# Optimization experiments

Measured on AMD Instinct MI355X. Metric: run time of the kernel, lower is better.

Reference implementation:

```python
import jax, jax.numpy as jnp
import numpy as np
from jax.scipy.linalg import solve_triangular

EPS = 2e-05  # module eps (only used on Cholesky failure in torch; cov is PD here since M >> N)


def setup_inputs() -> dict:
    key = jax.random.key(0)
    k1, k2, k3 = jax.random.split(key, 3)
    B, N, H, W = 8, 512, 64, 64
    return {
        "cont_feat": jax.random.normal(k1, (B, N, H, W), dtype=jnp.float32),
        "styl_feat": jax.random.normal(k2, (B, N, H, W), dtype=jnp.float32),
        "x_real": jax.random.normal(k3, (B, N, H, W), dtype=jnp.float32),
    }


def reference(cont_feat, styl_feat, x_real):
    B, N, cH, cW = cont_feat.shape
    xc = cont_feat.reshape(B, N, -1)   # [B, N, Mc]
    xs = styl_feat.reshape(B, N, -1)   # [B, N, Ms]
    # x_real is reshaped in the original but never used by whitening()

    # whitening: center, covariance, Cholesky, inv(L) @ x (as triangular solve)
    xc_c = xc - jnp.mean(xc, axis=-1, keepdims=True)
    cov_c = jnp.einsum('bnm,bkm->bnk', xc_c, xc_c) / (xc_c.shape[-1] - 1)  # [B,N,N]
    Lc = jnp.linalg.cholesky(cov_c)
    whiten = solve_triangular(Lc, xc_c, lower=True)  # == inv(Lc) @ xc_c

    # coloring: style covariance Cholesky, Ls @ whiten + style mean
    xs_mean = jnp.mean(xs, axis=-1, keepdims=True)
    xs_c = xs - xs_mean
    cov_s = jnp.einsum('bnm,bkm->bnk', xs_c, xs_c) / (xs_c.shape[-1] - 1)
    Ls = jnp.linalg.cholesky(cov_s)
    out = jnp.einsum('bnk,bkm->bnm', Ls, whiten) + xs_mean
    return out.reshape(B, N, cH, cW)
```

## Files before the change

kernel.cpp:

```cpp
#include <hip/hip_runtime.h>
#include <stdint.h>


using short8   = __attribute__((ext_vector_type(8))) short;
using short4_t = __attribute__((ext_vector_type(4))) short;
using f32x4    = __attribute__((ext_vector_type(4))) float;

#define DEVI static __device__ __forceinline__

DEVI uint16_t f32_to_bf16(float f) {
  union { float f; uint32_t u; } v{f};
  uint32_t u = v.u;
  return (uint16_t)((u + 0x7fffu + ((u >> 16) & 1u)) >> 16);
}

DEVI f32x4 mfma16(short8 a, short8 b, f32x4 c) {
  return __builtin_amdgcn_mfma_f32_16x16x32_bf16(a, b, c, 0, 0, 0);
}

typedef __attribute__((address_space(3))) uint32_t lds_u32;
typedef __attribute__((address_space(1))) const uint32_t gmem_u32;

DEVI void async_cp16(const uint16_t* g, uint16_t* l) {
  __builtin_amdgcn_global_load_lds((gmem_u32*)g, (lds_u32*)l, 16, 0, 0);
}

DEVI void stage_tile(const uint16_t* __restrict__ src, int stride,
                     uint16_t* lds, int tid) {
  int w64 = (tid >> 6) << 6;
  #pragma unroll
  for (int i = 0; i < 4; ++i) {
    int f = i * 256 + tid;
    int r = f >> 3, s = f & 7;
    int c = s ^ (r & 7);
    async_cp16(src + r * stride + c * 8, lds + (i * 256 + w64) * 8);
  }
}

DEVI short8 frag_ld(const uint16_t* lds, int r, int ch) {
  return *(const short8*)(lds + r * 64 + ((ch ^ (r & 7)) * 8));
}

__global__ __launch_bounds__(256) void k_meanconv(
    const float* __restrict__ cont, const float* __restrict__ styl,
    uint16_t* __restrict__ Yc, uint16_t* __restrict__ Ys, float* __restrict__ mus) {
  int rid = blockIdx.x;
  int row = rid & 4095;
  bool is_s = rid >= 4096;
  const float* src = (is_s ? styl : cont) + (size_t)row * 4096;
  uint16_t* dst = (is_s ? Ys : Yc) + (size_t)row * 4096;
  int tid = threadIdx.x, lane = tid & 63, w = tid >> 6;

  float4 v[4];
  #pragma unroll
  for (int i = 0; i < 4; ++i) v[i] = ((const float4*)src)[i * 256 + tid];
  float s = 0.f;
  #pragma unroll
  for (int i = 0; i < 4; ++i) s += v[i].x + v[i].y + v[i].z + v[i].w;
  #pragma unroll
  for (int off = 32; off > 0; off >>= 1) s += __shfl_down(s, off);
  __shared__ float red[4];
  if (lane == 0) red[w] = s;
  __syncthreads();
  float mean = (red[0] + red[1] + red[2] + red[3]) * (1.0f / 4096.0f);
  if (is_s && tid == 0) mus[row] = mean;

  #pragma unroll
  for (int i = 0; i < 4; ++i) {
    short4_t o;
    o[0] = (short)f32_to_bf16(v[i].x - mean);
    o[1] = (short)f32_to_bf16(v[i].y - mean);
    o[2] = (short)f32_to_bf16(v[i].z - mean);
    o[3] = (short)f32_to_bf16(v[i].w - mean);
    ((short4_t*)dst)[i * 256 + tid] = o;
  }
}

__global__ __launch_bounds__(256) void k_covp(const uint16_t* __restrict__ Y,
                                              float* __restrict__ covA,
                                              float* __restrict__ covB) {
  int bx = blockIdx.x;
  int split = bx & 1, rest = bx >> 1;
  int mat = rest / 10, q = rest % 10;
  int it = (q >= 6) ? 3 : (q >= 3) ? 2 : (q >= 1) ? 1 : 0;
  int jt = q - it * (it + 1) / 2;
  const uint16_t* A = Y + (size_t)mat * 2097152;
  float* C = covA + (size_t)mat * 262144;
  __shared__ uint16_t Al[128 * 64], Bl[128 * 64];
  int tid = threadIdx.x, lane = tid & 63, w = tid >> 6;
  int wr = w >> 1, wc = w & 1, m16 = lane & 15, q4 = lane >> 4;

  f32x4 acc[4][4] = {};
  for (int kb = split * 32; kb < split * 32 + 32; ++kb) {
    __syncthreads();
    stage_tile(A + it * 128 * 4096 + kb * 64, 4096, Al, tid);
    stage_tile(A + jt * 128 * 4096 + kb * 64, 4096, Bl, tid);
    __syncthreads();
    #pragma unroll
    for (int ks = 0; ks < 2; ++ks) {
      short8 af[4], bg[4];
      #pragma unroll
      for (int t = 0; t < 4; ++t) af[t] = frag_ld(Al, wr * 64 + t * 16 + m16, ks * 4 + q4);
      #pragma unroll
      for (int t = 0; t < 4; ++t) bg[t] = frag_ld(Bl, wc * 64 + t * 16 + m16, ks * 4 + q4);
      #pragma unroll
      for (int i2 = 0; i2 < 4; ++i2)
        #pragma unroll
        for (int j2 = 0; j2 < 4; ++j2)
          acc[i2][j2] = mfma16(af[i2], bg[j2], acc[i2][j2]);
    }
  }
  const float sc = 1.0f / 4095.0f;
  if (split == 0) {
    #pragma unroll
    for (int t = 0; t < 4; ++t)
      #pragma unroll
      for (int u = 0; u < 4; ++u)
        #pragma unroll
        for (int g = 0; g < 4; ++g) {
          int row = it * 128 + wr * 64 + t * 16 + q4 * 4 + g;
          int col = jt * 128 + wc * 64 + u * 16 + m16;
          C[row * 512 + col] = acc[t][u][g] * sc;
        }
  } else {
    float* Bp = covB + (size_t)rest * 16384;
    #pragma unroll
    for (int t = 0; t < 4; ++t)
      #pragma unroll
      for (int u = 0; u < 4; ++u)
        #pragma unroll
        for (int g = 0; g < 4; ++g) {
          int row = wr * 64 + t * 16 + q4 * 4 + g;
          int col = wc * 64 + u * 16 + m16;
          Bp[row * 128 + col] = acc[t][u][g] * sc;
        }
  }
}

__global__ __launch_bounds__(256) void k_covfix(float* __restrict__ covA,
                                                const float* __restrict__ covB) {
  int bx = blockIdx.x;
  int mat = bx / 10, q = bx % 10;
  int it = (q >= 6) ? 3 : (q >= 3) ? 2 : (q >= 1) ? 1 : 0;
  int jt = q - it * (it + 1) / 2;
  float* C = covA + (size_t)mat * 262144;
  const float* Bp = covB + (size_t)bx * 16384;
  for (int e = threadIdx.x; e < 16384; e += 256) {
    int r = e >> 7, c = e & 127;
    C[(it * 128 + r) * 512 + jt * 128 + c] += Bp[e];
  }
}

__global__ __launch_bounds__(512) void k_chol(float* __restrict__ covA,
                                              uint16_t* __restrict__ L16) {
  int mat = blockIdx.x;
  float* C = covA + (size_t)mat * 262144;
  uint16_t* L = L16 + (size_t)mat * 262144;
  __shared__ float P[512 * 36];
  __shared__ uint16_t Pb[512 * 40];
  __shared__ uint16_t Mb[32 * 40];
  int tid = threadIdx.x, lane = tid & 63, w = tid >> 6;
  int m16 = lane & 15, q4 = lane >> 4;

  for (int j = 0; j < 16; ++j) {
    int c0 = j * 32, n = 512 - c0;

    for (int e = tid; e < n * 8; e += 512) {
      int r = e >> 3, c4 = e & 7;
      *(float4*)&P[r * 36 + c4 * 4] =
          *(const float4*)(C + (size_t)(c0 + r) * 512 + c0 + c4 * 4);
    }
    __syncthreads();

    if (w == 0) {
      if (c0 > 0) {
        f32x4 t00 = {}, t10 = {}, t11 = {};
        const uint16_t* L0  = L + (size_t)(c0 + m16) * 512 + q4 * 8;
        const uint16_t* L1r = L + (size_t)(c0 + 16 + m16) * 512 + q4 * 8;
        short8 f0 = *(const short8*)(L0);
        short8 f1 = *(const short8*)(L1r);
        for (int kk = 0; kk < c0; kk += 32) {
          int kn = (kk + 32 < c0) ? kk + 32 : kk;
          short8 g0 = *(const short8*)(L0 + kn);
          short8 g1 = *(const short8*)(L1r + kn);
          t00 = mfma16(f0, f0, t00);
          t10 = mfma16(f1, f0, t10);
          t11 = mfma16(f1, f1, t11);
          f0 = g0; f1 = g1;
        }
        #pragma unroll
        for (int g = 0; g < 4; ++g) {
          int r0 = q4 * 4 + g;
          P[r0 * 36 + m16]              -= t00[g];
          P[(16 + r0) * 36 + m16]       -= t10[g];
          P[(16 + r0) * 36 + 16 + m16]  -= t11[g];
        }
      }
      if (lane < 32) {
        int r = lane;
        float a[32];
        #pragma unroll
        for (int c4 = 0; c4 < 8; ++c4) {
          float4 v = *(const float4*)&P[r * 36 + c4 * 4];
          a[c4 * 4 + 0] = v.x; a[c4 * 4 + 1] = v.y;
          a[c4 * 4 + 2] = v.z; a[c4 * 4 + 3] = v.w;
        }
        float myinv = 0.f;
        #pragma unroll
        for (int t = 0; t < 32; ++t) {
          float pv  = __shfl(a[t], t);
          float inv = __builtin_amdgcn_rsqf(pv);
          a[t] *= inv;
          if (r == t) myinv = inv;
          float scv = a[t];
          #pragma unroll
          for (int c = t + 1; c < 32; ++c)
            a[c] -= scv * __shfl(scv, c);
        }
        float xv[32];
        #pragma unroll
        for (int c = 0; c < 32; ++c) xv[c] = (c <= r) ? a[c] : 0.0f;
        float* Cw = C + (size_t)(c0 + r) * 512 + c0;
        uint16_t* Lw = L + (size_t)(c0 + r) * 512 + c0;
        #pragma unroll
        for (int c4 = 0; c4 < 8; ++c4)
          *(float4*)(Cw + c4 * 4) = make_float4(xv[c4 * 4], xv[c4 * 4 + 1],
                                                xv[c4 * 4 + 2], xv[c4 * 4 + 3]);
        #pragma unroll
        for (int c8 = 0; c8 < 4; ++c8) {
          short8 o;
          #pragma unroll
          for (int u = 0; u < 8; ++u) o[u] = (short)f32_to_bf16(xv[c8 * 8 + u]);
          *(short8*)(Lw + c8 * 8) = o;
        }
        if (n > 32) {
          float b[32];
          #pragma unroll
          for (int c = 0; c < 32; ++c) b[c] = (c == r) ? myinv : 0.0f;
          #pragma unroll
          for (int m = 0; m < 31; ++m) {
            float coef = a[m] * myinv;
            #pragma unroll
            for (int c = 0; c <= m; ++c) {
              float v = __shfl(b[c], m);
              if (r > m) b[c] -= coef * v;
            }
          }
          uint16_t* Mw = Mb + r * 40;
          #pragma unroll
          for (int c8 = 0; c8 < 4; ++c8) {
            short8 o;
            #pragma unroll
            for (int u = 0; u < 8; ++u) o[u] = (short)f32_to_bf16(b[c8 * 8 + u]);
            *(short8*)(Mw + c8 * 8) = o;
          }
        }
      }
    } else {
      int ntiles = (n - 32) >> 4;
      const uint16_t* B0 = L + (size_t)(c0 + m16) * 512 + q4 * 8;
      const uint16_t* B1 = L + (size_t)(c0 + 16 + m16) * 512 + q4 * 8;
      for (int t = w - 1; t < ntiles; t += 7) {
        f32x4 acc0 = {}, acc1 = {};
        const uint16_t* Ar = L + (size_t)(c0 + 32 + t * 16 + m16) * 512 + q4 * 8;
        if (c0 > 0) {
          short8 af = *(const short8*)(Ar);
          short8 b0 = *(const short8*)(B0);
          short8 b1 = *(const short8*)(B1);
          for (int kk = 0; kk < c0; kk += 32) {
            int kn = (kk + 32 < c0) ? kk + 32 : kk;
            short8 nf = *(const short8*)(Ar + kn);
            short8 n0 = *(const short8*)(B0 + kn);
            short8 n1 = *(const short8*)(B1 + kn);
            acc0 = mfma16(af, b0, acc0);
            acc1 = mfma16(af, b1, acc1);
            af = nf; b0 = n0; b1 = n1;
          }
        }
        #pragma unroll
        for (int g = 0; g < 4; ++g) {
          int pr = 32 + t * 16 + q4 * 4 + g;
          float v0 = P[pr * 36 + m16]      - acc0[g];
          float v1 = P[pr * 36 + 16 + m16] - acc1[g];
          Pb[pr * 40 + m16]      = f32_to_bf16(v0);
          Pb[pr * 40 + 16 + m16] = f32_to_bf16(v1);
        }
      }
    }
    __syncthreads();

    if (n > 32) {
      int ntiles = (n - 32) >> 4;
      short8 bm0 = *(const short8*)(Mb + m16 * 40 + q4 * 8);
      short8 bm1 = *(const short8*)(Mb + (16 + m16) * 40 + q4 * 8);
      for (int t = w; t < ntiles; t += 8) {
        short8 af = *(const short8*)(Pb + (size_t)(32 + t * 16 + m16) * 40 + q4 * 8);
        f32x4 x0 = {}, x1 = {};
        x0 = mfma16(af, bm0, x0);
        x1 = mfma16(af, bm1, x1);
        #pragma unroll
        for (int g = 0; g < 4; ++g) {
          int gr = c0 + 32 + t * 16 + q4 * 4 + g;
          float v0 = x0[g], v1 = x1[g];
          C[(size_t)gr * 512 + c0 + m16]      = v0;
          C[(size_t)gr * 512 + c0 + 16 + m16] = v1;
          L[(size_t)gr * 512 + c0 + m16]      = f32_to_bf16(v0);
          L[(size_t)gr * 512 + c0 + 16 + m16] = f32_to_bf16(v1);
        }
      }
    }
  }
}

__global__ __launch_bounds__(256) void k_trinv(const float* __restrict__ covA,
                                               uint16_t* __restrict__ Ut) {
  int bx = blockIdx.x;
  int matb = bx >> 5;
  int sub = bx & 31;
  int cb = sub >> 2, colgrp = sub & 3;
  const float* Lm = covA + (size_t)matb * 262144;
  uint16_t* U = Ut + (size_t)matb * 262144;
  int tid = threadIdx.x, lane = tid & 63, w = tid >> 6;
  int j = cb * 64 + colgrp * 16 + w * 4;

  __shared__ float Bl[64 * 66];
  __shared__ float Xl[4][4][512];

  for (int rb = cb; rb < 8; ++rb) {
    float acc[4];
    #pragma unroll
    for (int c = 0; c < 4; ++c) acc[c] = ((rb * 64 + lane) == (j + c)) ? 1.0f : 0.0f;
    for (int pb = cb; pb < rb; ++pb) {
      __syncthreads();
      for (int e = tid; e < 4096; e += 256)
        Bl[(e >> 6) * 66 + (e & 63)] = Lm[(rb * 64 + (e >> 6)) * 512 + pb * 64 + (e & 63)];
      __syncthreads();
      #pragma unroll 4
      for (int m = 0; m < 64; m += 2) {
        float2 b2 = *(const float2*)&Bl[lane * 66 + m];
        #pragma unroll
        for (int c = 0; c < 4; ++c)
          acc[c] -= b2.x * Xl[w][c][pb * 64 + m] + b2.y * Xl[w][c][pb * 64 + m + 1];
      }
    }
    __syncthreads();
    for (int e = tid; e < 4096; e += 256)
      Bl[(e >> 6) * 66 + (e & 63)] = Lm[(rb * 64 + (e >> 6)) * 512 + rb * 64 + (e & 63)];
    __syncthreads();
    float invd = __builtin_amdgcn_rcpf(Bl[lane * 66 + lane]);
    #pragma unroll 1
    for (int i = 0; i < 64; ++i) {
      float bcol = Bl[lane * 66 + i];
      if (lane == i) {
        #pragma unroll
        for (int c = 0; c < 4; ++c) acc[c] *= invd;
      }
      float xi[4];
      #pragma unroll
      for (int c = 0; c < 4; ++c) xi[c] = __shfl(acc[c], i);
      if (lane > i) {
        #pragma unroll
        for (int c = 0; c < 4; ++c) acc[c] -= bcol * xi[c];
      }
    }
    #pragma unroll
    for (int c = 0; c < 4; ++c) {
      Xl[w][c][rb * 64 + lane] = acc[c];
      U[(j + c) * 512 + rb * 64 + lane] = f32_to_bf16(acc[c]);
    }
  }
}

__global__ __launch_bounds__(256) void k_tprod(const uint16_t* __restrict__ Ls16,
                                               const uint16_t* __restrict__ Ut16,
                                               uint16_t* __restrict__ T16) {
  int bx = blockIdx.x;
  int b = bx / 10, q = bx % 10;
  int it = (q >= 6) ? 3 : (q >= 3) ? 2 : (q >= 1) ? 1 : 0;
  int jt = q - it * (it + 1) / 2;
  const uint16_t* A = Ls16 + (size_t)b * 262144;
  const uint16_t* B = Ut16 + (size_t)b * 262144;
  uint16_t* C = T16 + (size_t)b * 262144;
  __shared__ uint16_t Al[128 * 64], Bl[128 * 64];
  int tid = threadIdx.x, lane = tid & 63, w = tid >> 6;
  int wr = w >> 1, wc = w & 1, m16 = lane & 15, q4 = lane >> 4;

  f32x4 acc[4][4] = {};
  for (int kb = jt * 2; kb < (it + 1) * 2; ++kb) {
    __syncthreads();
    stage_tile(A + it * 128 * 512 + kb * 64, 512, Al, tid);
    stage_tile(B + jt * 128 * 512 + kb * 64, 512, Bl, tid);
    __syncthreads();
    #pragma unroll
    for (int ks = 0; ks < 2; ++ks) {
      short8 af[4], bg[4];
      #pragma unroll
      for (int t = 0; t < 4; ++t) af[t] = frag_ld(Al, wr * 64 + t * 16 + m16, ks * 4 + q4);
      #pragma unroll
      for (int t = 0; t < 4; ++t) bg[t] = frag_ld(Bl, wc * 64 + t * 16 + m16, ks * 4 + q4);
      #pragma unroll
      for (int i2 = 0; i2 < 4; ++i2)
        #pragma unroll
        for (int j2 = 0; j2 < 4; ++j2)
          acc[i2][j2] = mfma16(af[i2], bg[j2], acc[i2][j2]);
    }
  }
  #pragma unroll
  for (int t = 0; t < 4; ++t)
    #pragma unroll
    for (int u = 0; u < 4; ++u)
      #pragma unroll
      for (int g = 0; g < 4; ++g) {
        int row = it * 128 + wr * 64 + t * 16 + q4 * 4 + g;
        int col = jt * 128 + wc * 64 + u * 16 + m16;
        C[row * 512 + col] = f32_to_bf16(acc[t][u][g]);
      }
}

__global__ __launch_bounds__(256) void k_out(const uint16_t* __restrict__ T16,
                                             const uint16_t* __restrict__ Ycb,
                                             const float* __restrict__ mus,
                                             float* __restrict__ out) {
  int bx = blockIdx.x;
  int b = bx >> 7, q = bx & 127;
  int it = q >> 5, mt = q & 31;
  int m0 = mt * 128;
  const uint16_t* Tm = T16 + (size_t)b * 262144;
  const uint16_t* Y = Ycb + (size_t)b * 2097152;
  __shared__ uint16_t Al[128 * 64];
  __shared__ uint16_t Bt[128 * 68];
  int tid = threadIdx.x, lane = tid & 63, w = tid >> 6;
  int wr = w >> 1, wc = w & 1, m16 = lane & 15, q4 = lane >> 4;

  f32x4 acc[4][4] = {};
  int kbmax = (it + 1) * 2;
  for (int kb = 0; kb < kbmax; ++kb) {
    __syncthreads();
    stage_tile(Tm + it * 128 * 512 + kb * 64, 512, Al, tid);
    #pragma unroll
    for (int rep = 0; rep < 2; ++rep) {
      int task = rep * 256 + tid;
      int n8 = task & 15, kp = task >> 4;
      const uint16_t* p = Y + (size_t)(kb * 64 + 2 * kp) * 4096 + m0 + n8 * 8;
      short8 a0 = *(const short8*)p;
      short8 a1 = *(const short8*)(p + 4096);
      #pragma unroll
      for (int u = 0; u < 8; ++u) {
        int n = n8 * 8 + u;
        uint32_t pk = (uint32_t)(uint16_t)a0[u] | ((uint32_t)(uint16_t)a1[u] << 16);
        *(uint32_t*)(Bt + n * 68 + 2 * kp) = pk;
      }
    }
    __syncthreads();
    #pragma unroll
    for (int ks = 0; ks < 2; ++ks) {
      short8 af[4], bg[4];
      #pragma unroll
      for (int t = 0; t < 4; ++t) af[t] = frag_ld(Al, wr * 64 + t * 16 + m16, ks * 4 + q4);
      #pragma unroll
      for (int t = 0; t < 4; ++t) {
        int n = wc * 64 + t * 16 + m16;
        int ko = ks * 4 + q4;
        short8 bb;
        ((short4_t*)&bb)[0] = *(const short4_t*)(Bt + n * 68 + ko * 8);
        ((short4_t*)&bb)[1] = *(const short4_t*)(Bt + n * 68 + ko * 8 + 4);
        bg[t] = bb;
      }
      #pragma unroll
      for (int i2 = 0; i2 < 4; ++i2)
        #pragma unroll
        for (int j2 = 0; j2 < 4; ++j2)
          acc[i2][j2] = mfma16(af[i2], bg[j2], acc[i2][j2]);
    }
  }
  #pragma unroll
  for (int t = 0; t < 4; ++t)
    #pragma unroll
    for (int g = 0; g < 4; ++g) {
      int row = it * 128 + wr * 64 + t * 16 + q4 * 4 + g;
      float mu = mus[b * 512 + row];
      #pragma unroll
      for (int u = 0; u < 4; ++u) {
        int col = m0 + wc * 64 + u * 16 + m16;
        out[(size_t)(b * 512 + row) * 4096 + col] = acc[t][u][g] + mu;
      }
    }
}

extern "C" void kernel_launch(void* const* d_in, const int* in_sizes, int n_in,
                              void* d_out, int out_size, void* d_ws, size_t ws_size,
                              hipStream_t stream) {
  const float* cont = (const float*)d_in[0];
  const float* styl = (const float*)d_in[1];
  float* out = (float*)d_out;
  char* ws = (char*)d_ws;

  uint16_t* Ycb  = (uint16_t*)(ws);
  float*    covA = (float*)(ws + 67108864);
  uint16_t* L16  = (uint16_t*)(ws + 83886080);
  uint16_t* Ut16 = (uint16_t*)(ws + 92274688);
  uint16_t* T16  = (uint16_t*)(ws + 96468992);
  float*    mus  = (float*)(ws + 100663296);
  float*    covB = (float*)(ws + 83886080);

  uint16_t* Ysb  = Ycb + 16777216;
  uint16_t* Ls16 = L16 + 8 * 262144;

  k_meanconv<<<dim3(8192), dim3(256), 0, stream>>>(cont, styl, Ycb, Ysb, mus);
  k_covp    <<<dim3(320),  dim3(256), 0, stream>>>(Ycb, covA, covB);
  k_covfix  <<<dim3(160),  dim3(256), 0, stream>>>(covA, covB);
  hipMemsetAsync((void*)L16, 0, 16777216, stream);
  k_chol    <<<dim3(16),   dim3(512), 0, stream>>>(covA, L16);
  k_trinv   <<<dim3(256),  dim3(256), 0, stream>>>(covA, Ut16);
  k_tprod   <<<dim3(80),   dim3(256), 0, stream>>>(Ls16, Ut16, T16);
  k_out     <<<dim3(1024), dim3(256), 0, stream>>>(T16, Ycb, mus, out);
}
```

Before: 736.1 us.

## Stage Cholesky panel rows of L in LDS and deepen trailing-update prefetch

In the blocked Cholesky kernel, the 32 panel rows of the bf16 L factor are copied into a shared-memory buffer once per panel step. The diagonal and off-diagonal update loops then read B operands from LDS instead of repeatedly re-reading global memory across waves. The off-diagonal loop is also restructured to prefetch four A chunks ahead in registers, and a trailing barrier is added to protect the new buffer. This costs about 33KB more LDS per block and one extra sync per iteration.

Result: faster. 703.1 us (-4.5%).

```diff
diff --git a/kernel.cpp b/kernel.cpp
--- a/kernel.cpp
+++ b/kernel.cpp
@@ -158,6 +158,7 @@
   uint16_t* L = L16 + (size_t)mat * 262144;
   __shared__ float P[512 * 36];
   __shared__ uint16_t Pb[512 * 40];
+  __shared__ uint16_t Bb[32 * 520];
   __shared__ uint16_t Mb[32 * 40];
   int tid = threadIdx.x, lane = tid & 63, w = tid >> 6;
   int m16 = lane & 15, q4 = lane >> 4;
@@ -170,23 +171,26 @@
       *(float4*)&P[r * 36 + c4 * 4] =
           *(const float4*)(C + (size_t)(c0 + r) * 512 + c0 + c4 * 4);
     }
+    if (c0 > 0) {
+      int cpr = c0 >> 3;
+      for (int e = tid; e < 32 * cpr; e += 512) {
+        int r = e / cpr, cc = e - r * cpr;
+        *(short8*)(Bb + r * 520 + cc * 8) =
+            *(const short8*)(L + (size_t)(c0 + r) * 512 + cc * 8);
+      }
+    }
     __syncthreads();
 
     if (w == 0) {
       if (c0 > 0) {
         f32x4 t00 = {}, t10 = {}, t11 = {};
-        const uint16_t* L0  = L + (size_t)(c0 + m16) * 512 + q4 * 8;
-        const uint16_t* L1r = L + (size_t)(c0 + 16 + m16) * 512 + q4 * 8;
-        short8 f0 = *(const short8*)(L0);
-        short8 f1 = *(const short8*)(L1r);
+        #pragma unroll 4
         for (int kk = 0; kk < c0; kk += 32) {
-          int kn = (kk + 32 < c0) ? kk + 32 : kk;
-          short8 g0 = *(const short8*)(L0 + kn);
-          short8 g1 = *(const short8*)(L1r + kn);
+          short8 f0 = *(const short8*)(Bb + m16 * 520 + kk + q4 * 8);
+          short8 f1 = *(const short8*)(Bb + (16 + m16) * 520 + kk + q4 * 8);
           t00 = mfma16(f0, f0, t00);
           t10 = mfma16(f1, f0, t10);
           t11 = mfma16(f1, f1, t11);
-          f0 = g0; f1 = g1;
         }
         #pragma unroll
         for (int g = 0; g < 4; ++g) {
@@ -258,24 +262,29 @@
       }
     } else {
       int ntiles = (n - 32) >> 4;
-      const uint16_t* B0 = L + (size_t)(c0 + m16) * 512 + q4 * 8;
-      const uint16_t* B1 = L + (size_t)(c0 + 16 + m16) * 512 + q4 * 8;
       for (int t = w - 1; t < ntiles; t += 7) {
         f32x4 acc0 = {}, acc1 = {};
         const uint16_t* Ar = L + (size_t)(c0 + 32 + t * 16 + m16) * 512 + q4 * 8;
         if (c0 > 0) {
-          short8 af = *(const short8*)(Ar);
-          short8 b0 = *(const short8*)(B0);
-          short8 b1 = *(const short8*)(B1);
-          for (int kk = 0; kk < c0; kk += 32) {
-            int kn = (kk + 32 < c0) ? kk + 32 : kk;
-            short8 nf = *(const short8*)(Ar + kn);
-            short8 n0 = *(const short8*)(B0 + kn);
-            short8 n1 = *(const short8*)(B1 + kn);
-            acc0 = mfma16(af, b0, acc0);
-            acc1 = mfma16(af, b1, acc1);
-            af = nf; b0 = n0; b1 = n1;
+#define LDA(dst, kidx) { int ko_ = ((kidx) < c0) ? (kidx) : 0; \
+                         dst = *(const short8*)(Ar + ko_); }
+#define STEPK(areg, koff) if ((kb + (koff)) < c0) { \
+    int kk2 = kb + (koff); \
+    short8 b0_ = *(const short8*)(Bb + m16 * 520 + kk2 + q4 * 8); \
+    short8 b1_ = *(const short8*)(Bb + (16 + m16) * 520 + kk2 + q4 * 8); \
+    acc0 = mfma16(areg, b0_, acc0); \
+    acc1 = mfma16(areg, b1_, acc1); }
+          short8 a0, a1, a2, a3, p0, p1, p2, p3;
+          LDA(p0, 0) LDA(p1, 32) LDA(p2, 64) LDA(p3, 96)
+          int nch = (j + 3) >> 2;
+          for (int ch = 0; ch < nch; ++ch) {
+            int kb = ch * 128, kn2 = kb + 128;
+            a0 = p0; a1 = p1; a2 = p2; a3 = p3;
+            LDA(p0, kn2) LDA(p1, kn2 + 32) LDA(p2, kn2 + 64) LDA(p3, kn2 + 96)
+            STEPK(a0, 0) STEPK(a1, 32) STEPK(a2, 64) STEPK(a3, 96)
           }
+#undef LDA
+#undef STEPK
         }
         #pragma unroll
         for (int g = 0; g < 4; ++g) {
@@ -309,6 +318,7 @@
         }
       }
     }
+    __syncthreads();
   }
 }
 
```
